# Performance work log

Measured on AMD Instinct MI355X. Metric: run time of the kernel, lower is better.

## Reference

```python
import jax, jax.numpy as jnp
import numpy as np

D_MODEL = 1024
NUM_HEADS = 16
D_K = D_MODEL // NUM_HEADS
THETA = 10000.0


def _rope(x, pos):
    # x: [B, H, T, d_k], pos: [T]
    inv_freq = 1.0 / (THETA ** (jnp.arange(0, D_K, 2, dtype=jnp.float32) / D_K))  # [d_k/2]
    ang = pos.astype(jnp.float32)[:, None] * inv_freq[None, :]                    # [T, d_k/2]
    cos = jnp.repeat(jnp.cos(ang), 2, axis=-1)                                    # [T, d_k]
    sin = jnp.repeat(jnp.sin(ang), 2, axis=-1)
    x = x.astype(jnp.float32)
    x0 = x[..., ::2]
    x1 = x[..., 1::2]
    rot = jnp.stack((-x1, x0), axis=-1).reshape(x.shape)  # rotate_half, interleaved
    return x * cos + rot * sin


def setup_inputs() -> dict:
    key = jax.random.key(0)
    k1, k2, k3 = jax.random.split(key, 3)
    B, T = 2, 2048
    sigma_qkv = float(np.sqrt(2.0 / (D_MODEL + 3 * D_MODEL)))
    sigma_out = float(np.sqrt(2.0 / (D_MODEL + D_MODEL)))
    return {
        "x": jax.random.normal(k1, (B, T, D_MODEL), dtype=jnp.float32),
        "w_qkv": jax.random.normal(k2, (3 * D_MODEL, D_MODEL), dtype=jnp.float32) * sigma_qkv,
        "w_out": jax.random.normal(k3, (D_MODEL, D_MODEL), dtype=jnp.float32) * sigma_out,
    }


def reference(x, w_qkv, w_out):
    B, T, _ = x.shape
    qkv = jnp.einsum("btd,ed->bte", x, w_qkv)                 # [B, T, 3*D]
    q, k, v = jnp.split(qkv, 3, axis=-1)

    def split_head(t):
        return t.reshape(B, T, NUM_HEADS, D_K).transpose(0, 2, 1, 3)  # [B, H, T, d_k]

    q, k, v = split_head(q), split_head(k), split_head(v)
    pos = jnp.arange(T)
    q = _rope(q, pos)
    k = _rope(k, pos)

    scores = jnp.einsum("bhqd,bhkd->bhqk", q, k) / jnp.sqrt(jnp.float32(D_K))
    causal = jnp.tril(jnp.ones((T, T), dtype=bool))            # True = keep
    scores = jnp.where(causal[None, None], scores, -jnp.inf)
    attn = jax.nn.softmax(scores, axis=-1)
    out = jnp.einsum("bhqk,bhkd->bhqd", attn, v)               # [B, H, T, d_k]
    out = out.transpose(0, 2, 1, 3).reshape(B, T, D_MODEL)
    return jnp.einsum("btd,ed->bte", out, w_out)
```

## Files before the change

kernel.cpp:

```cpp
#include <hip/hip_runtime.h>
#include <cstdint>
#include <cstddef>

#define BB 2
#define TT 2048
#define DMODEL 1024
#define NHEADS 16
#define DK 64

typedef short short8 __attribute__((ext_vector_type(8)));
typedef unsigned short ushort8 __attribute__((ext_vector_type(8)));
typedef float floatx4 __attribute__((ext_vector_type(4)));
typedef _Float16 half4 __attribute__((ext_vector_type(4)));

#define MFMA_PV(A, B, C) __builtin_amdgcn_mfma_f32_16x16x16f16(A, B, C, 0, 0, 0)

__device__ __forceinline__ unsigned short f2bf(float f) {
    uint32_t u = __builtin_bit_cast(uint32_t, f);
    uint32_t r = (u + 0x7FFFu + ((u >> 16) & 1u)) >> 16;
    return (unsigned short)r;
}
__device__ __forceinline__ float bf2f(unsigned short s) {
    uint32_t u = ((uint32_t)s) << 16;
    return __builtin_bit_cast(float, u);
}

#define GLDS16(g, l) __builtin_amdgcn_global_load_lds( \
    (const __attribute__((address_space(1))) void*)(g), \
    (__attribute__((address_space(3))) void*)(l), 16, 0, 0)

__global__ void castk3(const float* __restrict__ x, unsigned short* __restrict__ xb,
                       const float* __restrict__ wq, unsigned short* __restrict__ wqb,
                       const float* __restrict__ wo, unsigned short* __restrict__ wob) {
    int bid = blockIdx.x;
    const float* in;
    unsigned short* out;
    int base;
    if (bid < 4096)       { in = x;  out = xb;  base = bid * 1024; }
    else if (bid < 7168)  { in = wq; out = wqb; base = (bid - 4096) * 1024; }
    else                  { in = wo; out = wob; base = (bid - 7168) * 1024; }
    int i = base + threadIdx.x * 4;
    float4 v = *(const float4*)(in + i);
    ushort4 o;
    o.x = f2bf(v.x); o.y = f2bf(v.y); o.z = f2bf(v.z); o.w = f2bf(v.w);
    *(ushort4*)(out + i) = o;
}

template <typename OUT>
__global__ __launch_bounds__(256)
void gemm_bt(const unsigned short* __restrict__ A, const unsigned short* __restrict__ B,
             OUT* __restrict__ C, int M, int N, int K) {
    __shared__ unsigned short As[128 * 32];
    __shared__ unsigned short Bs[128 * 32];

    const int tid  = threadIdx.x;
    const int lane = tid & 63;
    const int w    = tid >> 6;
    const int wm   = w & 1;
    const int wn   = w >> 1;
    const int quad = lane >> 4;
    const int l16  = lane & 15;

    const int m0 = blockIdx.y * 128;
    const int n0 = blockIdx.x * 128;

    floatx4 acc[4][4];
#pragma unroll
    for (int a = 0; a < 4; a++)
#pragma unroll
        for (int b = 0; b < 4; b++)
            acc[a][b] = (floatx4){0.f, 0.f, 0.f, 0.f};

    const int c0 = w * 128 + lane;
    const int c1 = c0 + 64;
    const int r0 = c0 >> 2, cc0 = (c0 & 3) ^ ((r0 >> 1) & 3);
    const int r1 = c1 >> 2, cc1 = (c1 & 3) ^ ((r1 >> 1) & 3);

    const unsigned short* gA0 = A + (size_t)(m0 + r0) * K + cc0 * 8;
    const unsigned short* gA1 = A + (size_t)(m0 + r1) * K + cc1 * 8;
    const unsigned short* gB0 = B + (size_t)(n0 + r0) * K + cc0 * 8;
    const unsigned short* gB1 = B + (size_t)(n0 + r1) * K + cc1 * 8;

    unsigned short* lA0 = &As[(2 * w + 0) * 512];
    unsigned short* lA1 = &As[(2 * w + 1) * 512];
    unsigned short* lB0 = &Bs[(2 * w + 0) * 512];
    unsigned short* lB1 = &Bs[(2 * w + 1) * 512];

    const int rsw = (l16 >> 1) & 3;

    for (int k0 = 0; k0 < K; k0 += 32) {
        __syncthreads();
        GLDS16(gA0 + k0, lA0);
        GLDS16(gA1 + k0, lA1);
        GLDS16(gB0 + k0, lB0);
        GLDS16(gB1 + k0, lB1);
        __syncthreads();

        short8 af[4], bf[4];
#pragma unroll
        for (int t = 0; t < 4; t++) {
            af[t] = *(const short8*)&As[(wm * 64 + t * 16 + l16) * 32 + (quad ^ rsw) * 8];
            bf[t] = *(const short8*)&Bs[(wn * 64 + t * 16 + l16) * 32 + (quad ^ rsw) * 8];
        }
#pragma unroll
        for (int tm = 0; tm < 4; tm++)
#pragma unroll
            for (int tn = 0; tn < 4; tn++)
                acc[tm][tn] = __builtin_amdgcn_mfma_f32_16x16x32_bf16(
                    af[tm], bf[tn], acc[tm][tn], 0, 0, 0);
    }

#pragma unroll
    for (int tm = 0; tm < 4; tm++) {
#pragma unroll
        for (int tn = 0; tn < 4; tn++) {
#pragma unroll
            for (int r = 0; r < 4; r++) {
                int m = m0 + wm * 64 + tm * 16 + quad * 4 + r;
                int n = n0 + wn * 64 + tn * 16 + l16;
                if constexpr (sizeof(OUT) == 4)
                    C[(size_t)m * N + n] = acc[tm][tn][r];
                else
                    C[(size_t)m * N + n] = f2bf(acc[tm][tn][r]);
            }
        }
    }
}

__global__ __launch_bounds__(256)
void ropevt(const unsigned short* __restrict__ qkv,
            unsigned short* __restrict__ qb, unsigned short* __restrict__ kb,
            unsigned short* __restrict__ vtb) {
    __shared__ unsigned short tile[64][72];
    const int tid = threadIdx.x;
    const int bh  = blockIdx.y;
    const int b = bh >> 4, h = bh & 15;
    const int t0 = blockIdx.x * 64;

    const float QS = 0.18033688f;
#pragma unroll
    for (int rep = 0; rep < 8; rep++) {
        int idx  = rep * 256 + tid;
        int p    = idx & 31;
        int trow = idx >> 5;
        int t    = t0 + trow;

        size_t src = (size_t)(b * TT + t) * 3072 + h * 64 + 2 * p;
        ushort2 qu = *(const ushort2*)(qkv + src);
        ushort2 ku = *(const ushort2*)(qkv + src + 1024);
        float qx = bf2f(qu.x), qy = bf2f(qu.y);
        float kx = bf2f(ku.x), ky = bf2f(ku.y);

        float invf = __powf(10000.f, -((float)(2 * p)) / 64.f);
        float ang  = (float)t * invf;
        float sn, cs;
        __sincosf(ang, &sn, &cs);

        size_t dst = ((size_t)bh * TT + t) * 64 + 2 * p;
        ushort2 qo, ko;
        qo.x = f2bf((qx * cs - qy * sn) * QS); qo.y = f2bf((qy * cs + qx * sn) * QS);
        ko.x = f2bf(kx * cs - ky * sn); ko.y = f2bf(ky * cs + kx * sn);
        *(ushort2*)(qb + dst) = qo;
        *(ushort2*)(kb + dst) = ko;
    }

    const int row = tid >> 2;
    const unsigned short* src = qkv + ((size_t)(b * TT) + t0 + row) * 3072 + 2048 + h * 64;
    {
        int cb = (tid & 3) * 16;
        ushort8 v0 = *(const ushort8*)(src + cb);
        ushort8 v1 = *(const ushort8*)(src + cb + 8);
#pragma unroll
        for (int i = 0; i < 8; i++) tile[row][cb + i] = v0[i];
#pragma unroll
        for (int i = 0; i < 8; i++) tile[row][cb + 8 + i] = v1[i];
    }
    __syncthreads();

    const int d  = tid >> 2;
    const int tc = tid & 3;
    const int hs = (d & 1) * 4;
    ushort8 o0, o1;
#pragma unroll
    for (int i = 0; i < 8; i++) {
        _Float16 hv = (_Float16)bf2f(tile[tc * 16 + (i ^ hs)][d]);
        o0[i] = __builtin_bit_cast(unsigned short, hv);
    }
#pragma unroll
    for (int i = 0; i < 8; i++) {
        _Float16 hv = (_Float16)bf2f(tile[tc * 16 + 8 + (i ^ hs)][d]);
        o1[i] = __builtin_bit_cast(unsigned short, hv);
    }
    unsigned short* dst = vtb + ((size_t)bh * 64 + d) * TT + t0 + tc * 16;
    *(ushort8*)(dst) = o0;
    *(ushort8*)(dst + 8) = o1;
}

__global__ __launch_bounds__(256, 5)
void attn_mfma(const unsigned short* __restrict__ qb,
               const unsigned short* __restrict__ kb,
               const unsigned short* __restrict__ vtb,
               unsigned short* __restrict__ out) {
    __shared__ unsigned short Ks[2][64 * 64];
    __shared__ unsigned short Vs[2][64 * 64];

    const int tid  = threadIdx.x;
    const int lane = tid & 63;
    const int w    = tid >> 6;
    const int quad = lane >> 4;
    const int l16  = lane & 15;

    const int bh    = blockIdx.x;
    const int qtile = gridDim.y - 1 - blockIdx.y;
    const int q0    = qtile * 64;

    const unsigned short* Qp = qb + ((size_t)bh * TT + q0 + w * 16) * 64;
    const unsigned short* Kp = kb + (size_t)bh * TT * 64;
    const unsigned short* Vp = vtb + (size_t)bh * 64 * TT;

    short8 aq[2];
#pragma unroll
    for (int ks = 0; ks < 2; ks++)
        aq[ks] = *(const short8*)(Qp + (size_t)l16 * 64 + ks * 32 + quad * 8);

    floatx4 Oacc[4];
#pragma unroll
    for (int dt = 0; dt < 4; dt++) Oacc[dt] = (floatx4){0.f, 0.f, 0.f, 0.f};
    float m = -1e30f, l = 0.f;

    const int ntiles = qtile + 1;

#define STAGE(IT, P)                                                                      \
    {                                                                                     \
        const int j0s = (IT) * 64;                                                        \
        _Pragma("unroll")                                                                 \
        for (int rep = 0; rep < 2; rep++) {                                               \
            int c    = rep * 256 + tid;                                                   \
            int row  = c >> 3, sl = c & 7;                                                \
            GLDS16(Kp + (size_t)(j0s + row) * 64 + (sl ^ (row & 7)) * 8, &Ks[P][c * 8]);  \
            GLDS16(Vp + (size_t)row * TT + j0s + (sl ^ ((row >> 1) & 7)) * 8,             \
                   &Vs[P][c * 8]);                                                        \
        }                                                                                 \
    }

    STAGE(0, 0);
    __syncthreads();

    const int ksw = l16 & 7;
    const int vsw = (l16 >> 1) & 7;
    const int vsub = ((quad & 1) ^ (l16 & 1)) * 4;

    for (int it = 0; it < ntiles; ++it) {
        const int p = it & 1;
        if (it + 1 < ntiles) STAGE(it + 1, p ^ 1);

        floatx4 sacc[4];
#pragma unroll
        for (int nt = 0; nt < 4; nt++) sacc[nt] = (floatx4){0.f, 0.f, 0.f, 0.f};
#pragma unroll
        for (int ks = 0; ks < 2; ks++)
#pragma unroll
            for (int nt = 0; nt < 4; nt++) {
                short8 kf = *(const short8*)&Ks[p][(nt * 16 + l16) * 64 + ((ks * 4 + quad) ^ ksw) * 8];
                sacc[nt] = __builtin_amdgcn_mfma_f32_16x16x32_bf16(kf, aq[ks], sacc[nt], 0, 0, 0);
            }

        if (it == qtile) {
            const int qg = w * 16 + l16;
#pragma unroll
            for (int nt = 0; nt < 4; nt++)
#pragma unroll
                for (int r = 0; r < 4; r++)
                    if (nt * 16 + quad * 4 + r > qg) sacc[nt][r] = -1e30f;
        }

        float mx = sacc[0][0];
#pragma unroll
        for (int nt = 0; nt < 4; nt++)
#pragma unroll
            for (int r = 0; r < 4; r++) mx = fmaxf(mx, sacc[nt][r]);
        mx = fmaxf(mx, __shfl_xor(mx, 16));
        mx = fmaxf(mx, __shfl_xor(mx, 32));
        float mnew  = fmaxf(m, mx);
        float alpha = __builtin_amdgcn_exp2f(m - mnew);
        m = mnew;
        float psum = 0.f;
#pragma unroll
        for (int nt = 0; nt < 4; nt++)
#pragma unroll
            for (int r = 0; r < 4; r++) {
                float pv = __builtin_amdgcn_exp2f(sacc[nt][r] - mnew);
                sacc[nt][r] = pv;
                psum += pv;
            }
        psum += __shfl_xor(psum, 16);
        psum += __shfl_xor(psum, 32);
        l = l * alpha + psum;

#pragma unroll
        for (int dt = 0; dt < 4; dt++)
#pragma unroll
            for (int r = 0; r < 4; r++) Oacc[dt][r] *= alpha;

        half4 bp[4];
#pragma unroll
        for (int nt = 0; nt < 4; nt++) {
            half4 h;
            h[0] = (_Float16)sacc[nt][0];
            h[1] = (_Float16)sacc[nt][1];
            h[2] = (_Float16)sacc[nt][2];
            h[3] = (_Float16)sacc[nt][3];
            bp[nt] = h;
        }

#pragma unroll
        for (int dt = 0; dt < 4; dt++)
#pragma unroll
            for (int nt = 0; nt < 4; nt++) {
                int c = nt * 2 + (quad >> 1);
                half4 vf = *(const half4*)&Vs[p][(dt * 16 + l16) * 64 + (c ^ vsw) * 8 + vsub];
                Oacc[dt] = MFMA_PV(vf, bp[nt], Oacc[dt]);
            }

        __syncthreads();
    }
#undef STAGE

    const int b = bh >> 4, h = bh & 15;
    const float inv = 1.f / l;
    const size_t base = ((size_t)(b * TT + q0 + w * 16 + l16)) * DMODEL + h * 64 + quad * 4;
#pragma unroll
    for (int dt = 0; dt < 4; dt++) {
        ushort4 pk;
        pk.x = f2bf(Oacc[dt][0] * inv);
        pk.y = f2bf(Oacc[dt][1] * inv);
        pk.z = f2bf(Oacc[dt][2] * inv);
        pk.w = f2bf(Oacc[dt][3] * inv);
        *(ushort4*)(out + base + dt * 16) = pk;
    }
}

extern "C" void kernel_launch(void* const* d_in, const int* in_sizes, int n_in,
                              void* d_out, int out_size, void* d_ws, size_t ws_size,
                              hipStream_t stream) {
    const float* x     = (const float*)d_in[0];
    const float* w_qkv = (const float*)d_in[1];
    const float* w_out = (const float*)d_in[2];
    float* out = (float*)d_out;

    char* ws = (char*)d_ws;

    unsigned short* xb   = (unsigned short*)(ws);
    unsigned short* wqb  = (unsigned short*)(ws + 8388608);
    unsigned short* wob  = (unsigned short*)(ws + 14680064);
    unsigned short* qkvb = (unsigned short*)(ws + 16777216);
    unsigned short* qb   = (unsigned short*)(ws + 41943040);
    unsigned short* kb   = (unsigned short*)(ws + 50331648);
    unsigned short* vtb  = (unsigned short*)(ws + 58720256);
    unsigned short* attb = (unsigned short*)(ws + 67108864);

    castk3<<<8192, 256, 0, stream>>>(x, xb, w_qkv, wqb, w_out, wob);

    gemm_bt<unsigned short><<<dim3(3072 / 128, 4096 / 128), 256, 0, stream>>>(
        xb, wqb, qkvb, 4096, 3072, 1024);

    ropevt<<<dim3(TT / 64, BB * NHEADS), 256, 0, stream>>>(qkvb, qb, kb, vtb);

    attn_mfma<<<dim3(BB * NHEADS, TT / 64), 256, 0, stream>>>(qb, kb, vtb, attb);

    gemm_bt<float><<<dim3(1024 / 128, 4096 / 128), 256, 0, stream>>>(
        attb, wob, out, 4096, 1024, 1024);
}
```

Before: 192.4 us.

## Use 256x256-tile 4-stage pipelined GEMM for QKV projection

Replaces the 128x128 QKV projection GEMM with a new 512-thread kernel that computes 256x256 output tiles. It uses a 4-stage shared-memory ring fed by direct global-to-LDS loads, a swizzled LDS layout, split A/B staging interleaved with MFMA phases, and s_setprio around the MFMA blocks. The goal is more data reuse per block and better overlap of loads with matrix math. The cost is 128KB of LDS and a grid of only 192 blocks, so occupancy is one block per CU and some CUs sit idle at the tail.

Measured after the change: 196.4 us. 2.1% more time.

```diff
diff --git a/kernel.cpp b/kernel.cpp
--- a/kernel.cpp
+++ b/kernel.cpp
@@ -127,6 +127,127 @@
     }
 }
 
+__global__ __launch_bounds__(512)
+void gemm256(const unsigned short* __restrict__ A, const unsigned short* __restrict__ B,
+             unsigned short* __restrict__ C, int M, int N, int K) {
+    __shared__ unsigned short As[4][8192];
+    __shared__ unsigned short Bs[4][8192];
+
+    const int tid  = threadIdx.x;
+    const int lane = tid & 63;
+    const int w    = tid >> 6;
+    const int wm   = w >> 2;
+    const int wn   = w & 3;
+    const int quad = lane >> 4;
+    const int l16  = lane & 15;
+
+    const int m0 = blockIdx.y * 256;
+    const int n0 = blockIdx.x * 256;
+
+    floatx4 acc[8][4];
+#pragma unroll
+    for (int a = 0; a < 8; a++)
+#pragma unroll
+        for (int b = 0; b < 4; b++)
+            acc[a][b] = (floatx4){0.f, 0.f, 0.f, 0.f};
+
+    const int rA = tid >> 2;
+    const int cA = (tid & 3) ^ ((tid >> 3) & 3);
+    const unsigned short* gA0 = A + (size_t)(m0 + rA) * K + cA * 8;
+    const unsigned short* gA1 = gA0 + (size_t)128 * K;
+    const unsigned short* gB0 = B + (size_t)(n0 + rA) * K + cA * 8;
+    const unsigned short* gB1 = gB0 + (size_t)128 * K;
+
+    const int NT = K >> 5;
+
+    GLDS16(gA0,      &As[0][w * 512]);
+    GLDS16(gA1,      &As[0][4096 + w * 512]);
+    GLDS16(gB0,      &Bs[0][w * 512]);
+    GLDS16(gB1,      &Bs[0][4096 + w * 512]);
+    GLDS16(gA0 + 32, &As[1][w * 512]);
+    GLDS16(gA1 + 32, &As[1][4096 + w * 512]);
+    GLDS16(gB0 + 32, &Bs[1][w * 512]);
+    GLDS16(gB1 + 32, &Bs[1][4096 + w * 512]);
+    GLDS16(gA0 + 64, &As[2][w * 512]);
+    GLDS16(gA1 + 64, &As[2][4096 + w * 512]);
+    GLDS16(gB0 + 64, &Bs[2][w * 512]);
+    GLDS16(gB1 + 64, &Bs[2][4096 + w * 512]);
+    asm volatile("s_waitcnt vmcnt(8)" ::: "memory");
+    __builtin_amdgcn_s_barrier();
+
+    const int rsw  = (l16 >> 1) & 3;
+    const int aoff = (wm * 128 + l16) * 32 + ((quad ^ rsw) * 8);
+    const int boff = (wn * 64  + l16) * 32 + ((quad ^ rsw) * 8);
+
+#define TILE_BODY(IT, DO_STAGE, VMWAIT)                                         \
+    {                                                                           \
+        const int s_ = (IT) & 3;                                                \
+        short8 bfr[4], afr[4];                                                  \
+        _Pragma("unroll")                                                       \
+        for (int nf = 0; nf < 4; nf++)                                          \
+            bfr[nf] = *(const short8*)&Bs[s_][boff + nf * 512];                 \
+        _Pragma("unroll")                                                       \
+        for (int mf = 0; mf < 4; mf++)                                          \
+            afr[mf] = *(const short8*)&As[s_][aoff + mf * 512];                 \
+        if (DO_STAGE) {                                                         \
+            const int sn_ = ((IT) + 3) & 3;                                     \
+            GLDS16(gA0 + ((IT) + 3) * 32, &As[sn_][w * 512]);                   \
+            GLDS16(gA1 + ((IT) + 3) * 32, &As[sn_][4096 + w * 512]);            \
+        }                                                                       \
+        __builtin_amdgcn_s_barrier();                                           \
+        asm volatile("s_waitcnt lgkmcnt(0)" ::: "memory");                      \
+        __builtin_amdgcn_s_setprio(1);                                          \
+        _Pragma("unroll")                                                       \
+        for (int mf = 0; mf < 4; mf++)                                          \
+            _Pragma("unroll")                                                   \
+            for (int nf = 0; nf < 4; nf++)                                      \
+                acc[mf][nf] = __builtin_amdgcn_mfma_f32_16x16x32_bf16(          \
+                    afr[mf], bfr[nf], acc[mf][nf], 0, 0, 0);                    \
+        __builtin_amdgcn_s_setprio(0);                                          \
+        __builtin_amdgcn_s_barrier();                                           \
+        _Pragma("unroll")                                                       \
+        for (int mf = 0; mf < 4; mf++)                                          \
+            afr[mf] = *(const short8*)&As[s_][aoff + (4 + mf) * 512];           \
+        if (DO_STAGE) {                                                         \
+            const int sn_ = ((IT) + 3) & 3;                                     \
+            GLDS16(gB0 + ((IT) + 3) * 32, &Bs[sn_][w * 512]);                   \
+            GLDS16(gB1 + ((IT) + 3) * 32, &Bs[sn_][4096 + w * 512]);            \
+        }                                                                       \
+        asm volatile(VMWAIT ::: "memory");                                      \
+        __builtin_amdgcn_s_barrier();                                           \
+        asm volatile("s_waitcnt lgkmcnt(0)" ::: "memory");                      \
+        __builtin_amdgcn_s_setprio(1);                                          \
+        _Pragma("unroll")                                                       \
+        for (int mf = 0; mf < 4; mf++)                                          \
+            _Pragma("unroll")                                                   \
+            for (int nf = 0; nf < 4; nf++)                                      \
+                acc[4 + mf][nf] = __builtin_amdgcn_mfma_f32_16x16x32_bf16(      \
+                    afr[mf], bfr[nf], acc[4 + mf][nf], 0, 0, 0);                \
+        __builtin_amdgcn_s_setprio(0);                                          \
+        __builtin_amdgcn_s_barrier();                                           \
+    }
+
+    for (int it = 0; it < NT - 3; ++it)
+        TILE_BODY(it, 1, "s_waitcnt vmcnt(8)");
+    TILE_BODY(NT - 3, 0, "s_waitcnt vmcnt(4)");
+    TILE_BODY(NT - 2, 0, "s_waitcnt vmcnt(0)");
+    TILE_BODY(NT - 1, 0, "s_waitcnt vmcnt(0)");
+#undef TILE_BODY
+
+#pragma unroll
+    for (int mf = 0; mf < 8; mf++) {
+#pragma unroll
+        for (int nf = 0; nf < 4; nf++) {
+#pragma unroll
+            for (int r = 0; r < 4; r++) {
+                int m = m0 + wm * 128 + mf * 16 + quad * 4 + r;
+                int n = n0 + wn * 64 + nf * 16 + l16;
+                C[(size_t)m * N + n] = f2bf(acc[mf][nf][r]);
+            }
+        }
+    }
+}
+
 __global__ __launch_bounds__(256)
 void ropevt(const unsigned short* __restrict__ qkv,
             unsigned short* __restrict__ qb, unsigned short* __restrict__ kb,
@@ -361,7 +482,7 @@
 
     castk3<<<8192, 256, 0, stream>>>(x, xb, w_qkv, wqb, w_out, wob);
 
-    gemm_bt<unsigned short><<<dim3(3072 / 128, 4096 / 128), 256, 0, stream>>>(
+    gemm256<<<dim3(3072 / 256, 4096 / 256), 512, 0, stream>>>(
         xb, wqb, qkvb, 4096, 3072, 1024);
 
     ropevt<<<dim3(TT / 64, BB * NHEADS), 256, 0, stream>>>(qkvb, qb, kb, vtb);
```

## Add 256x256 pipelined QKV GEMM and triple-buffer attention K/V loads

Applied to the files above, without the earlier changes.

Replaces the 128x128 QKV projection GEMM with a new 512-thread 256x256 tile kernel. The new kernel double-buffers A and B halves with direct global-to-LDS loads, swizzles workgroup order across XCDs, and raises wave priority around the MFMA bursts. The attention kernel moves from double to triple buffering of K/V tiles, using explicit vmcnt waits and raw barriers in place of __syncthreads. The goal is more load/compute overlap and more reuse per block. The cost is extra LDS, which drops the attention occupancy hint from 5 to 3, and the large GEMM tile gives only 192 blocks.

After: 188.3 us. 1.02x faster.

```diff
diff --git a/kernel.cpp b/kernel.cpp
--- a/kernel.cpp
+++ b/kernel.cpp
@@ -127,6 +127,160 @@
     }
 }
 
+__global__ __launch_bounds__(512)
+void gemm256(const unsigned short* __restrict__ A, const unsigned short* __restrict__ B,
+             unsigned short* __restrict__ C, int M, int N, int K) {
+    __shared__ unsigned short As[2][2][8192];
+    __shared__ unsigned short Bs[2][2][8192];
+
+    const int tid  = threadIdx.x;
+    const int lane = tid & 63;
+    const int w    = tid >> 6;
+    const int wm   = w >> 2;
+    const int wn   = w & 3;
+    const int quad = lane >> 4;
+    const int l16  = lane & 15;
+
+    const int gx  = gridDim.x;
+    const int bid = blockIdx.y * gx + blockIdx.x;
+    const int cpx = (gx * gridDim.y) >> 3;
+    const int wg  = (bid & 7) * cpx + (bid >> 3);
+    const int m0  = (wg / gx) * 256;
+    const int n0  = (wg % gx) * 256;
+
+    floatx4 acc[8][4];
+#pragma unroll
+    for (int a = 0; a < 8; a++)
+#pragma unroll
+        for (int b = 0; b < 4; b++)
+            acc[a][b] = (floatx4){0.f, 0.f, 0.f, 0.f};
+
+    const int r1   = tid >> 3;
+    const int koff = ((tid & 7) ^ (r1 & 7)) * 8;
+    const unsigned short* Ag = A + (size_t)(m0 + r1) * K + koff;
+    const unsigned short* Bg = B + (size_t)(n0 + r1) * K + koff;
+    const int NT2 = K >> 6;
+
+#define STAGE_A(dd, hh, kt) { \
+    GLDS16(Ag + (size_t)((hh) * 128) * K + (kt) * 64,      &As[dd][hh][tid * 8]); \
+    GLDS16(Ag + (size_t)((hh) * 128 + 64) * K + (kt) * 64, &As[dd][hh][4096 + tid * 8]); }
+#define STAGE_B(dd, hh, kt) { \
+    GLDS16(Bg + (size_t)((hh) * 128) * K + (kt) * 64,      &Bs[dd][hh][tid * 8]); \
+    GLDS16(Bg + (size_t)((hh) * 128 + 64) * K + (kt) * 64, &Bs[dd][hh][4096 + tid * 8]); }
+
+#define BARRIER() { __builtin_amdgcn_sched_barrier(0); __builtin_amdgcn_s_barrier(); \
+                    __builtin_amdgcn_sched_barrier(0); }
+
+    STAGE_B(0, 0, 0); STAGE_B(0, 1, 0);
+    STAGE_A(0, 0, 0); STAGE_A(0, 1, 0);
+    STAGE_B(1, 0, 1); STAGE_B(1, 1, 1);
+    asm volatile("s_waitcnt vmcnt(4)" ::: "memory");
+    BARRIER();
+
+    const int c0    = (quad ^ (l16 & 7)) * 8;
+    const int bhalf = wn >> 1;
+    const int brow0 = (wn & 1) * 64 + l16;
+
+    short8 a[8], b[8];
+
+    for (int it = 0; it < NT2; ++it) {
+        const int d = it & 1;
+
+#pragma unroll
+        for (int nfl = 0; nfl < 2; nfl++)
+#pragma unroll
+            for (int ks = 0; ks < 2; ks++)
+                b[2 * nfl + ks] = *(const short8*)&Bs[d][bhalf][(brow0 + nfl * 16) * 64 + (c0 ^ (ks * 32))];
+#pragma unroll
+        for (int mfl = 0; mfl < 4; mfl++)
+#pragma unroll
+            for (int ks = 0; ks < 2; ks++)
+                a[2 * mfl + ks] = *(const short8*)&As[d][wm][(l16 + mfl * 16) * 64 + (c0 ^ (ks * 32))];
+        if (it + 1 < NT2) STAGE_A(d ^ 1, 0, it + 1);
+        BARRIER();
+        __builtin_amdgcn_s_setprio(1);
+#pragma unroll
+        for (int mfl = 0; mfl < 4; mfl++)
+#pragma unroll
+            for (int nf = 0; nf < 2; nf++) {
+                acc[mfl][nf] = __builtin_amdgcn_mfma_f32_16x16x32_bf16(a[2 * mfl], b[2 * nf], acc[mfl][nf], 0, 0, 0);
+                acc[mfl][nf] = __builtin_amdgcn_mfma_f32_16x16x32_bf16(a[2 * mfl + 1], b[2 * nf + 1], acc[mfl][nf], 0, 0, 0);
+            }
+        __builtin_amdgcn_s_setprio(0);
+        BARRIER();
+
+#pragma unroll
+        for (int nfl = 0; nfl < 2; nfl++)
+#pragma unroll
+            for (int ks = 0; ks < 2; ks++)
+                b[4 + 2 * nfl + ks] = *(const short8*)&Bs[d][bhalf][(brow0 + 32 + nfl * 16) * 64 + (c0 ^ (ks * 32))];
+        if (it + 1 < NT2) STAGE_A(d ^ 1, 1, it + 1);
+        BARRIER();
+        __builtin_amdgcn_s_setprio(1);
+#pragma unroll
+        for (int mfl = 0; mfl < 4; mfl++)
+#pragma unroll
+            for (int nf = 2; nf < 4; nf++) {
+                acc[mfl][nf] = __builtin_amdgcn_mfma_f32_16x16x32_bf16(a[2 * mfl], b[2 * nf], acc[mfl][nf], 0, 0, 0);
+                acc[mfl][nf] = __builtin_amdgcn_mfma_f32_16x16x32_bf16(a[2 * mfl + 1], b[2 * nf + 1], acc[mfl][nf], 0, 0, 0);
+            }
+        __builtin_amdgcn_s_setprio(0);
+        BARRIER();
+
+#pragma unroll
+        for (int mfl = 0; mfl < 4; mfl++)
+#pragma unroll
+            for (int ks = 0; ks < 2; ks++)
+                a[2 * mfl + ks] = *(const short8*)&As[d][wm][(64 + l16 + mfl * 16) * 64 + (c0 ^ (ks * 32))];
+        if (it + 2 < NT2) STAGE_B(d, 0, it + 2);
+        BARRIER();
+        __builtin_amdgcn_s_setprio(1);
+#pragma unroll
+        for (int mfl = 0; mfl < 4; mfl++)
+#pragma unroll
+            for (int nf = 0; nf < 2; nf++) {
+                acc[4 + mfl][nf] = __builtin_amdgcn_mfma_f32_16x16x32_bf16(a[2 * mfl], b[2 * nf], acc[4 + mfl][nf], 0, 0, 0);
+                acc[4 + mfl][nf] = __builtin_amdgcn_mfma_f32_16x16x32_bf16(a[2 * mfl + 1], b[2 * nf + 1], acc[4 + mfl][nf], 0, 0, 0);
+            }
+        __builtin_amdgcn_s_setprio(0);
+        BARRIER();
+
+        if (it + 2 < NT2) STAGE_B(d, 1, it + 2);
+        if (it < NT2 - 2) {
+            asm volatile("s_waitcnt vmcnt(4)" ::: "memory");
+        } else if (it == NT2 - 2) {
+            asm volatile("s_waitcnt vmcnt(0)" ::: "memory");
+        }
+        BARRIER();
+        __builtin_amdgcn_s_setprio(1);
+#pragma unroll
+        for (int mfl = 0; mfl < 4; mfl++)
+#pragma unroll
+            for (int nf = 2; nf < 4; nf++) {
+                acc[4 + mfl][nf] = __builtin_amdgcn_mfma_f32_16x16x32_bf16(a[2 * mfl], b[2 * nf], acc[4 + mfl][nf], 0, 0, 0);
+                acc[4 + mfl][nf] = __builtin_amdgcn_mfma_f32_16x16x32_bf16(a[2 * mfl + 1], b[2 * nf + 1], acc[4 + mfl][nf], 0, 0, 0);
+            }
+        __builtin_amdgcn_s_setprio(0);
+        BARRIER();
+    }
+#undef STAGE_A
+#undef STAGE_B
+#undef BARRIER
+
+#pragma unroll
+    for (int mf = 0; mf < 8; mf++) {
+#pragma unroll
+        for (int nf = 0; nf < 4; nf++) {
+#pragma unroll
+            for (int r = 0; r < 4; r++) {
+                int m = m0 + wm * 128 + mf * 16 + quad * 4 + r;
+                int n = n0 + wn * 64 + nf * 16 + l16;
+                C[(size_t)m * N + n] = f2bf(acc[mf][nf][r]);
+            }
+        }
+    }
+}
+
 __global__ __launch_bounds__(256)
 void ropevt(const unsigned short* __restrict__ qkv,
             unsigned short* __restrict__ qb, unsigned short* __restrict__ kb,
@@ -196,13 +350,13 @@
     *(ushort8*)(dst + 8) = o1;
 }
 
-__global__ __launch_bounds__(256, 5)
+__global__ __launch_bounds__(256, 3)
 void attn_mfma(const unsigned short* __restrict__ qb,
                const unsigned short* __restrict__ kb,
                const unsigned short* __restrict__ vtb,
                unsigned short* __restrict__ out) {
-    __shared__ unsigned short Ks[2][64 * 64];
-    __shared__ unsigned short Vs[2][64 * 64];
+    __shared__ unsigned short Ks[3][64 * 64];
+    __shared__ unsigned short Vs[3][64 * 64];
 
     const int tid  = threadIdx.x;
     const int lane = tid & 63;
@@ -244,15 +398,22 @@
     }
 
     STAGE(0, 0);
-    __syncthreads();
+    if (ntiles > 1) {
+        STAGE(1, 1);
+        asm volatile("s_waitcnt vmcnt(4)" ::: "memory");
+    } else {
+        asm volatile("s_waitcnt vmcnt(0)" ::: "memory");
+    }
+    __builtin_amdgcn_s_barrier();
+    __builtin_amdgcn_sched_barrier(0);
 
     const int ksw = l16 & 7;
     const int vsw = (l16 >> 1) & 7;
     const int vsub = ((quad & 1) ^ (l16 & 1)) * 4;
 
     for (int it = 0; it < ntiles; ++it) {
-        const int p = it & 1;
-        if (it + 1 < ntiles) STAGE(it + 1, p ^ 1);
+        const int p = it % 3;
+        if (it + 2 < ntiles) STAGE(it + 2, (it + 2) % 3);
 
         floatx4 sacc[4];
 #pragma unroll
@@ -322,7 +483,15 @@
                 Oacc[dt] = MFMA_PV(vf, bp[nt], Oacc[dt]);
             }
 
-        __syncthreads();
+        if (it + 1 < ntiles) {
+            if (it + 2 < ntiles) {
+                asm volatile("s_waitcnt vmcnt(4)" ::: "memory");
+            } else {
+                asm volatile("s_waitcnt vmcnt(0)" ::: "memory");
+            }
+            __builtin_amdgcn_s_barrier();
+            __builtin_amdgcn_sched_barrier(0);
+        }
     }
 #undef STAGE
 
@@ -361,7 +530,7 @@
 
     castk3<<<8192, 256, 0, stream>>>(x, xb, w_qkv, wqb, w_out, wob);
 
-    gemm_bt<unsigned short><<<dim3(3072 / 128, 4096 / 128), 256, 0, stream>>>(
+    gemm256<<<dim3(3072 / 256, 4096 / 256), 512, 0, stream>>>(
         xb, wqb, qkvb, 4096, 3072, 1024);
 
     ropevt<<<dim3(TT / 64, BB * NHEADS), 256, 0, stream>>>(qkvb, qb, kb, vtb);
```
